# Kernel tuning notes

Hardware: AMD Instinct MI355X
Metric: run time of the kernel (lower is better)

## Reference

```python
import jax, jax.numpy as jnp
import numpy as np

B, G, DIN, DOUT = 4096, 16, 512, 512

def setup_inputs() -> dict:
    key = jax.random.key(0)
    kx, kw, kb = jax.random.split(key, 3)
    x = jax.random.normal(kx, (B, G, DIN), dtype=jnp.float32)
    # per-group nn.Linear weight: [G, dim_out, dim_in] (torch layout)
    W = jax.random.normal(kw, (G, DOUT, DIN), dtype=jnp.float32) * (1.0 / np.sqrt(DIN))
    b = jax.random.normal(kb, (G, DOUT), dtype=jnp.float32) * 0.01
    return {"x": x, "W": W, "b": b}

def reference(x, W, b):
    # MultiLinear: independent Linear per group g; y[..., g, :] = x[..., g, :] @ W[g].T + b[g]
    # Fused as a single batched GEMM over the group dimension.
    y = jnp.einsum('bgi,goi->bgo', x, W)  # [B, G, DOUT]
    return y + b
```

## Files before the change

kernel.cpp:

```cpp
#include <hip/hip_runtime.h>
#include <hip/hip_bf16.h>


#define BATCH 4096
#define NGRP  16
#define DIN   512
#define DOUT  512

#define BM 256
#define BN 256
#define BK 64
#define NT (DIN / BK)

typedef __bf16 bf16x8 __attribute__((ext_vector_type(8)));
typedef float  f32x4  __attribute__((ext_vector_type(4)));
typedef const __attribute__((address_space(1))) void gas_void;
typedef __attribute__((address_space(3))) void las_void;

__global__ __launch_bounds__(256)
void wcvt_kernel(const float* __restrict__ W, __bf16* __restrict__ Wb) {
    const int i = (blockIdx.x * 256 + threadIdx.x) * 8;
    f32x4 a = *(const f32x4*)(W + i);
    f32x4 b = *(const f32x4*)(W + i + 4);
    bf16x8 v;
#pragma unroll
    for (int j = 0; j < 4; ++j) { v[j] = (__bf16)a[j]; v[j + 4] = (__bf16)b[j]; }
    *(bf16x8*)(Wb + i) = v;
}

__global__ __launch_bounds__(512, 2)
void MultiLinear_48498770706571_kernel(const float* __restrict__ X,
                                       const __bf16* __restrict__ Wb,
                                       const float* __restrict__ Bias,
                                       float* __restrict__ Y) {
    const int bid = (blockIdx.x & 7) * 64 + (blockIdx.x >> 3);
    const int g   = bid >> 5;
    const int mt  = (bid >> 1) & 15;
    const int nt  = bid & 1;
    const int bm0 = mt * BM;
    const int bn0 = nt * BN;

    __shared__ __bf16 As[2][BM * BK];
    __shared__ __bf16 BsF[2][BN * BK];

    const int tid  = threadIdx.x;
    const int lane = tid & 63;
    const int w    = tid >> 6;
    const int wm   = (w >> 2) * 128;
    const int wn   = (w & 3) * 64;
    const int l15  = lane & 15;
    const int q    = lane >> 4;

    const int srow = tid >> 2;
    const int sc2  = (tid & 3) * 2;
    const float* pA = X + (size_t)(bm0 + srow) * (NGRP * DIN) + g * DIN + (tid & 3) * 16;
    const size_t strideA = (size_t)128 * (NGRP * DIN);

    const int drow0 = (w << 5) + (lane >> 3);
    const int dch   = lane & 7;
    const __bf16* wbase = Wb + (size_t)g * (DOUT * DIN) + (size_t)bn0 * DIN;

    f32x4 ra[2][4];

#define ISSUE_A(k0)                                                        \
    do {                                                                   \
        const f32x4* qa0 = (const f32x4*)(pA + (k0));                      \
        const f32x4* qa1 = (const f32x4*)(pA + strideA + (k0));            \
        ra[0][0] = qa0[0]; ra[0][1] = qa0[1]; ra[0][2] = qa0[2]; ra[0][3] = qa0[3]; \
        ra[1][0] = qa1[0]; ra[1][1] = qa1[1]; ra[1][2] = qa1[2]; ra[1][3] = qa1[3]; \
    } while (0)

#define CVT_WRITE_A(buf)                                                   \
    do {                                                                   \
        _Pragma("unroll")                                                  \
        for (int p = 0; p < 2; ++p) {                                      \
            bf16x8 v0, v1;                                                 \
            _Pragma("unroll")                                              \
            for (int j = 0; j < 4; ++j) {                                  \
                v0[j] = (__bf16)ra[p][0][j]; v0[j + 4] = (__bf16)ra[p][1][j]; \
                v1[j] = (__bf16)ra[p][2][j]; v1[j + 4] = (__bf16)ra[p][3][j]; \
            }                                                              \
            const int row = p * 128 + srow;                                \
            const int s   = srow & 7;                                      \
            __bf16* base = &As[buf][row * BK];                             \
            *(bf16x8*)&base[((sc2 ^ s) << 3)]       = v0;                  \
            *(bf16x8*)&base[(((sc2 + 1) ^ s) << 3)] = v1;                  \
        }                                                                  \
    } while (0)

#define DMA_B(kt, buf)                                                     \
    do {                                                                   \
        const size_t k0 = (size_t)(kt) * BK;                               \
        _Pragma("unroll")                                                  \
        for (int qq = 0; qq < 4; ++qq) {                                   \
            const int row = drow0 + (qq << 3);                             \
            const __bf16* gp = wbase + (size_t)row * DIN + k0              \
                               + ((dch ^ (row & 7)) << 3);                 \
            __builtin_amdgcn_global_load_lds(                              \
                (gas_void*)gp,                                             \
                (las_void*)&BsF[buf][(w << 11) + (qq << 9)], 16, 0, 0);    \
        }                                                                  \
    } while (0)

#define COMPUTE(buf)                                                       \
    do {                                                                   \
        _Pragma("unroll")                                                  \
        for (int kk = 0; kk < 2; ++kk) {                                   \
            bf16x8 af[8], bfr[4];                                          \
            _Pragma("unroll")                                              \
            for (int mi = 0; mi < 8; ++mi) {                               \
                const int row = wm + mi * 16 + l15;                        \
                const int ch  = ((kk << 2) + q) ^ (row & 7);               \
                af[mi] = *(const bf16x8*)&As[buf][row * BK + (ch << 3)];   \
            }                                                              \
            _Pragma("unroll")                                              \
            for (int ni = 0; ni < 4; ++ni) {                               \
                const int brow = wn + ni * 16 + l15;                       \
                const int ch = ((kk << 2) + q) ^ (brow & 7);               \
                bfr[ni] = *(const bf16x8*)&BsF[buf][brow * BK + (ch << 3)]; \
            }                                                              \
            _Pragma("unroll")                                              \
            for (int mi = 0; mi < 8; ++mi)                                 \
                _Pragma("unroll")                                          \
                for (int ni = 0; ni < 4; ++ni)                             \
                    acc[mi][ni] = __builtin_amdgcn_mfma_f32_16x16x32_bf16( \
                        af[mi], bfr[ni], acc[mi][ni], 0, 0, 0);            \
        }                                                                  \
    } while (0)

    f32x4 acc[8][4];
#pragma unroll
    for (int mi = 0; mi < 8; ++mi)
#pragma unroll
        for (int ni = 0; ni < 4; ++ni) acc[mi][ni] = f32x4{0.f, 0.f, 0.f, 0.f};

    ISSUE_A(0);
    DMA_B(0, 0);
    CVT_WRITE_A(0);
    ISSUE_A(BK);

    for (int kt = 0; kt < NT; ++kt) {
        const int cur = kt & 1;
        if (kt + 1 < NT)
            asm volatile("s_waitcnt vmcnt(8)" ::: "memory");
        else
            asm volatile("s_waitcnt vmcnt(0)" ::: "memory");
        asm volatile("s_waitcnt lgkmcnt(0)" ::: "memory");
        __builtin_amdgcn_s_barrier();

        if (kt + 1 < NT) DMA_B(kt + 1, cur ^ 1);

        COMPUTE(cur);

        if (kt + 1 < NT) {
            CVT_WRITE_A(cur ^ 1);
            if (kt + 2 < NT) ISSUE_A((kt + 2) * BK);
        }
    }

    const int r0 = (lane >> 4) * 4;
    const int c  = lane & 15;
    float bias_n[4];
#pragma unroll
    for (int ni = 0; ni < 4; ++ni)
        bias_n[ni] = Bias[g * DOUT + bn0 + wn + ni * 16 + c];
#pragma unroll
    for (int mi = 0; mi < 8; ++mi) {
#pragma unroll
        for (int j = 0; j < 4; ++j) {
            const int row = bm0 + wm + mi * 16 + r0 + j;
            float* yrow = Y + (size_t)row * (NGRP * DOUT) + g * DOUT + bn0 + wn;
#pragma unroll
            for (int ni = 0; ni < 4; ++ni)
                yrow[ni * 16 + c] = acc[mi][ni][j] + bias_n[ni];
        }
    }
#undef ISSUE_A
#undef CVT_WRITE_A
#undef DMA_B
#undef COMPUTE
}

extern "C" void kernel_launch(void* const* d_in, const int* in_sizes, int n_in,
                              void* d_out, int out_size, void* d_ws, size_t ws_size,
                              hipStream_t stream) {
    const float* X    = (const float*)d_in[0];
    const float* W    = (const float*)d_in[1];
    const float* Bias = (const float*)d_in[2];
    float* Y          = (float*)d_out;
    __bf16* Wb        = (__bf16*)d_ws;

    wcvt_kernel<<<2048, 256, 0, stream>>>(W, Wb);

    const int grid = NGRP * (BATCH / BM) * (DOUT / BN);
    MultiLinear_48498770706571_kernel<<<grid, 512, 0, stream>>>(X, Wb, Bias, Y);
}
```

Baseline: 86.47 us.

## Split main loop into four barrier-fenced phases with prioritized MFMA clusters

Restructures the K-loop into four phases per tile. Each phase reads a half-tile of A fragments (plus B fragments when needed), overlaps one piece of the next tile's global traffic (A load, B DMA to LDS, A convert/write), then runs a 4x4 MFMA cluster under raised wave priority (s_setprio). Fragment registers drop from af[8] to af[4], lowering VGPR pressure. In exchange the A prefetch distance shrinks from two tiles to one, and each iteration now has eight barriers, which can expose global-load latency and add sync overhead.

```diff
diff --git a/kernel.cpp b/kernel.cpp
--- a/kernel.cpp
+++ b/kernel.cpp
@@ -102,31 +102,40 @@
         }                                                                  \
     } while (0)
 
-#define COMPUTE(buf)                                                       \
-    do {                                                                   \
-        _Pragma("unroll")                                                  \
-        for (int kk = 0; kk < 2; ++kk) {                                   \
-            bf16x8 af[8], bfr[4];                                          \
+#define READ_AF(MLO, KK, buf)                                              \
+    do {                                                                   \
+        _Pragma("unroll")                                                  \
+        for (int mi = 0; mi < 4; ++mi) {                                   \
+            const int row = wm + ((MLO) + mi) * 16 + l15;                  \
+            const int ch  = (((KK) << 2) + q) ^ (row & 7);                 \
+            af[mi] = *(const bf16x8*)&As[buf][row * BK + (ch << 3)];       \
+        }                                                                  \
+    } while (0)
+
+#define READ_BF(KK, buf)                                                   \
+    do {                                                                   \
+        _Pragma("unroll")                                                  \
+        for (int ni = 0; ni < 4; ++ni) {                                   \
+            const int brow = wn + ni * 16 + l15;                           \
+            const int ch   = (((KK) << 2) + q) ^ (brow & 7);               \
+            bfr[ni] = *(const bf16x8*)&BsF[buf][brow * BK + (ch << 3)];    \
+        }                                                                  \
+    } while (0)
+
+#define MFMA_Q(MLO)                                                        \
+    do {                                                                   \
+        __builtin_amdgcn_s_setprio(1);                                     \
+        _Pragma("unroll")                                                  \
+        for (int mi = 0; mi < 4; ++mi)                                     \
             _Pragma("unroll")                                              \
-            for (int mi = 0; mi < 8; ++mi) {                               \
-                const int row = wm + mi * 16 + l15;                        \
-                const int ch  = ((kk << 2) + q) ^ (row & 7);               \
-                af[mi] = *(const bf16x8*)&As[buf][row * BK + (ch << 3)];   \
-            }                                                              \
-            _Pragma("unroll")                                              \
-            for (int ni = 0; ni < 4; ++ni) {                               \
-                const int brow = wn + ni * 16 + l15;                       \
-                const int ch = ((kk << 2) + q) ^ (brow & 7);               \
-                bfr[ni] = *(const bf16x8*)&BsF[buf][brow * BK + (ch << 3)]; \
-            }                                                              \
-            _Pragma("unroll")                                              \
-            for (int mi = 0; mi < 8; ++mi)                                 \
-                _Pragma("unroll")                                          \
-                for (int ni = 0; ni < 4; ++ni)                             \
-                    acc[mi][ni] = __builtin_amdgcn_mfma_f32_16x16x32_bf16( \
-                        af[mi], bfr[ni], acc[mi][ni], 0, 0, 0);            \
-        }                                                                  \
-    } while (0)
+            for (int ni = 0; ni < 4; ++ni)                                 \
+                acc[(MLO) + mi][ni] = __builtin_amdgcn_mfma_f32_16x16x32_bf16( \
+                    af[mi], bfr[ni], acc[(MLO) + mi][ni], 0, 0, 0);        \
+        __builtin_amdgcn_s_setprio(0);                                     \
+    } while (0)
+
+#define LGKM0() asm volatile("s_waitcnt lgkmcnt(0)" ::: "memory")
+#define BAR()   __builtin_amdgcn_s_barrier()
 
     f32x4 acc[8][4];
 #pragma unroll
@@ -137,25 +146,42 @@
     ISSUE_A(0);
     DMA_B(0, 0);
     CVT_WRITE_A(0);
-    ISSUE_A(BK);
+    asm volatile("s_waitcnt vmcnt(0)" ::: "memory");
+    LGKM0();
+    BAR();
 
     for (int kt = 0; kt < NT; ++kt) {
         const int cur = kt & 1;
-        if (kt + 1 < NT)
-            asm volatile("s_waitcnt vmcnt(8)" ::: "memory");
-        else
-            asm volatile("s_waitcnt vmcnt(0)" ::: "memory");
-        asm volatile("s_waitcnt lgkmcnt(0)" ::: "memory");
-        __builtin_amdgcn_s_barrier();
-
-        if (kt + 1 < NT) DMA_B(kt + 1, cur ^ 1);
-
-        COMPUTE(cur);
-
-        if (kt + 1 < NT) {
-            CVT_WRITE_A(cur ^ 1);
-            if (kt + 2 < NT) ISSUE_A((kt + 2) * BK);
-        }
+        const int nxt = cur ^ 1;
+        const bool pre = (kt + 1 < NT);
+        bf16x8 af[4], bfr[4];
+
+        READ_AF(0, 0, cur);
+        READ_BF(0, cur);
+        if (pre) ISSUE_A((kt + 1) * BK);
+        LGKM0(); BAR();
+        MFMA_Q(0);
+        BAR();
+
+        READ_AF(4, 0, cur);
+        if (pre) DMA_B(kt + 1, nxt);
+        LGKM0(); BAR();
+        MFMA_Q(4);
+        BAR();
+
+        READ_AF(0, 1, cur);
+        READ_BF(1, cur);
+        if (pre) CVT_WRITE_A(nxt);
+        LGKM0(); BAR();
+        MFMA_Q(0);
+        BAR();
+
+        READ_AF(4, 1, cur);
+        LGKM0();
+        if (pre) asm volatile("s_waitcnt vmcnt(0)" ::: "memory");
+        BAR();
+        MFMA_Q(4);
+        BAR();
     }
 
     const int r0 = (lane >> 4) * 4;
@@ -178,7 +204,11 @@
 #undef ISSUE_A
 #undef CVT_WRITE_A
 #undef DMA_B
-#undef COMPUTE
+#undef READ_AF
+#undef READ_BF
+#undef MFMA_Q
+#undef LGKM0
+#undef BAR
 }
 
 extern "C" void kernel_launch(void* const* d_in, const int* in_sizes, int n_in,
```

Result: slower. 89.82 us (+3.9%).
